# Performance work log

Hardware: AMD Instinct MI355X
Metric: run time of the kernel (lower is better)

The kernel has to match this reference:

```python
import jax, jax.numpy as jnp
import numpy as np

WIRE_DIM = 32
NUM_WIRES = 64
BATCH = 8192


def setup_inputs() -> dict:
    key = jax.random.key(0)
    k1, k2, k3, k4 = jax.random.split(key, 4)
    outputs = jax.random.normal(k1, (BATCH, NUM_WIRES * WIRE_DIM), dtype=jnp.float32)
    tests = jax.random.randint(k2, (BATCH, 2), 0, NUM_WIRES, dtype=jnp.int64)
    W1 = jax.random.normal(k3, (2 * WIRE_DIM, 10), dtype=jnp.float32) * 0.1
    b1 = jnp.zeros((10,), dtype=jnp.float32)
    W2 = jax.random.normal(k4, (10, 1), dtype=jnp.float32) * 0.1
    b2 = jnp.zeros((1,), dtype=jnp.float32)
    return {"outputs": outputs, "tests": tests, "W1": W1, "b1": b1, "W2": W2, "b2": b2}


def reference(outputs, tests, W1, b1, W2, b2):
    B = outputs.shape[0]
    W = outputs.shape[1] // WIRE_DIM          # num_wires
    wires = outputs.reshape(B, W, WIRE_DIM)   # [B, W, D]
    person = tests[:, 0]
    location = tests[:, 1]
    # gather_nd equivalent: person wire vector per batch element
    person_vec = wires[jnp.arange(B), person]                 # [B, D]
    # per-wire concat [person_vec, wire_vec] -> shared tiny MLP, vectorized over wires
    x = jnp.concatenate(
        [jnp.broadcast_to(person_vec[:, None, :], (B, W, WIRE_DIM)), wires], axis=-1
    )                                                          # [B, W, 2D]
    h = jax.nn.relu(jnp.einsum("bwd,dh->bwh", x, W1) + b1)     # [B, W, 10]
    logits = (jnp.einsum("bwh,ho->bwo", h, W2) + b2)[..., 0]   # [B, W]
    # sparse softmax cross entropy with location labels
    loss = -jnp.take_along_axis(jax.nn.log_softmax(logits, axis=-1),
                                location[:, None], axis=-1)[:, 0]  # [B]
    return loss
```

## Files before the change

kernel.cpp:

```cpp
#include <hip/hip_runtime.h>

#define WIRE_DIM  32
#define NUM_WIRES 64
#define BATCH     8192
#define HID       10
#define STRIDE    36

__device__ __forceinline__ float rl(float x, int slane) {
    return __uint_as_float(__builtin_amdgcn_readlane(__float_as_uint(x), slane));
}

__global__ __launch_bounds__(256) void isnet_kernel(
    const float* __restrict__ outputs,
    const int*   __restrict__ tests,
    const float* __restrict__ W1,
    const float* __restrict__ bias1,
    const float* __restrict__ W2,
    const float* __restrict__ bias2,
    float*       __restrict__ out)
{
    __shared__ __align__(16) float stage[4][NUM_WIRES * STRIDE];

    const int tid  = threadIdx.x;
    const int lane = tid & 63;
    const int wave = tid >> 6;
    float* buf = stage[wave];

    const int b = blockIdx.x * 4 + wave;

    const int sp = __builtin_amdgcn_readfirstlane(tests[2 * b]);
    const int sl = __builtin_amdgcn_readfirstlane(tests[2 * b + 1]);

    const int d  = lane & 31;
    const int h0 = (lane >> 5) * 5;
    float wp5[5];
    #pragma unroll
    for (int k = 0; k < 5; ++k) wp5[k] = W1[d * HID + h0 + k];

    const float* g = outputs + (size_t)b * (NUM_WIRES * WIRE_DIM) + lane * 4;
    const int r  = lane >> 3;
    const int cc = lane & 7;
    {
        float4 c[8];
        #pragma unroll
        for (int t = 0; t < 8; ++t) c[t] = *(const float4*)(g + t * 256);
        #pragma unroll
        for (int t = 0; t < 8; ++t)
            *(float4*)&buf[(t * 8 + r) * STRIDE + cc * 4] = c[t];
    }

    float pc[5];
    {
        const float pd = buf[sp * STRIDE + d];
        #pragma unroll
        for (int k = 0; k < 5; ++k) pc[k] = pd * wp5[k];
        #pragma unroll
        for (int off = 16; off > 0; off >>= 1)
            #pragma unroll
            for (int k = 0; k < 5; ++k) pc[k] += __shfl_xor(pc[k], off);
    }
    float pacc[HID];
    #pragma unroll
    for (int k = 0; k < 5; ++k) {
        pacc[k]     = rl(pc[k], 0);
        pacc[5 + k] = rl(pc[k], 32);
    }

    float4 x[8];
    #pragma unroll
    for (int t = 0; t < 8; ++t)
        x[t] = *(const float4*)&buf[lane * STRIDE + t * 4];

    float acc[HID];
    #pragma unroll
    for (int h = 0; h < HID; ++h) acc[h] = bias1[h] + pacc[h];

    #pragma unroll
    for (int j = 0; j < 8; ++j) {
        const float* ww = W1 + (32 + 4 * j) * HID;
        #pragma unroll
        for (int h = 0; h < HID; ++h) {
            acc[h] += x[j].x * ww[0 * HID + h] + x[j].y * ww[1 * HID + h]
                    + x[j].z * ww[2 * HID + h] + x[j].w * ww[3 * HID + h];
        }
    }

    float v = bias2[0];
    #pragma unroll
    for (int h = 0; h < HID; ++h) v += fmaxf(acc[h], 0.f) * W2[h];

    float m = v;
    #pragma unroll
    for (int off = 32; off > 0; off >>= 1) m = fmaxf(m, __shfl_xor(m, off));
    float s = __expf(v - m);
    #pragma unroll
    for (int off = 32; off > 0; off >>= 1) s += __shfl_xor(s, off);
    float lv = rl(v, sl);
    if (lane == 0) out[b] = m + __logf(s) - lv;
}

extern "C" void kernel_launch(void* const* d_in, const int* in_sizes, int n_in,
                              void* d_out, int out_size, void* d_ws, size_t ws_size,
                              hipStream_t stream) {
    const float* outputs = (const float*)d_in[0];
    const int*   tests   = (const int*)d_in[1];
    const float* W1      = (const float*)d_in[2];
    const float* b1      = (const float*)d_in[3];
    const float* W2      = (const float*)d_in[4];
    const float* b2      = (const float*)d_in[5];
    float* out = (float*)d_out;

    isnet_kernel<<<BATCH / 4, 256, 0, stream>>>(
        outputs, tests, W1, b1, W2, b2, out);
}
```

Baseline: 101.5 us.

## Process two batch rows per wave and drop softmax max-subtraction

```diff
diff --git a/kernel.cpp b/kernel.cpp
--- a/kernel.cpp
+++ b/kernel.cpp
@@ -26,10 +26,13 @@
     const int wave = tid >> 6;
     float* buf = stage[wave];
 
-    const int b = blockIdx.x * 4 + wave;
+    const int bA = blockIdx.x * 8 + wave * 2;
+    const int bB = bA + 1;
 
-    const int sp = __builtin_amdgcn_readfirstlane(tests[2 * b]);
-    const int sl = __builtin_amdgcn_readfirstlane(tests[2 * b + 1]);
+    const int spA = __builtin_amdgcn_readfirstlane(tests[2 * bA]);
+    const int slA = __builtin_amdgcn_readfirstlane(tests[2 * bA + 1]);
+    const int spB = __builtin_amdgcn_readfirstlane(tests[2 * bB]);
+    const int slB = __builtin_amdgcn_readfirstlane(tests[2 * bB + 1]);
 
     const int d  = lane & 31;
     const int h0 = (lane >> 5) * 5;
@@ -37,21 +40,29 @@
     #pragma unroll
     for (int k = 0; k < 5; ++k) wp5[k] = W1[d * HID + h0 + k];
 
-    const float* g = outputs + (size_t)b * (NUM_WIRES * WIRE_DIM) + lane * 4;
     const int r  = lane >> 3;
     const int cc = lane & 7;
-    {
-        float4 c[8];
-        #pragma unroll
-        for (int t = 0; t < 8; ++t) c[t] = *(const float4*)(g + t * 256);
-        #pragma unroll
-        for (int t = 0; t < 8; ++t)
-            *(float4*)&buf[(t * 8 + r) * STRIDE + cc * 4] = c[t];
-    }
+    const float* gA = outputs + (size_t)bA * (NUM_WIRES * WIRE_DIM) + lane * 4;
+    const float* gB = outputs + (size_t)bB * (NUM_WIRES * WIRE_DIM) + lane * 4;
+
+    float4 cA[8], cB[8];
+    #pragma unroll
+    for (int t = 0; t < 8; ++t) cA[t] = *(const float4*)(gA + t * 256);
+    #pragma unroll
+    for (int t = 0; t < 8; ++t) cB[t] = *(const float4*)(gB + t * 256);
+
+    #pragma unroll
+    for (int t = 0; t < 8; ++t)
+        *(float4*)&buf[(t * 8 + r) * STRIDE + cc * 4] = cA[t];
+
+    float4 x[8];
+    #pragma unroll
+    for (int t = 0; t < 8; ++t)
+        x[t] = *(const float4*)&buf[lane * STRIDE + t * 4];
 
     float pc[5];
     {
-        const float pd = buf[sp * STRIDE + d];
+        const float pd = buf[spA * STRIDE + d];
         #pragma unroll
         for (int k = 0; k < 5; ++k) pc[k] = pd * wp5[k];
         #pragma unroll
@@ -59,44 +70,69 @@
             #pragma unroll
             for (int k = 0; k < 5; ++k) pc[k] += __shfl_xor(pc[k], off);
     }
-    float pacc[HID];
+    float accA[HID];
     #pragma unroll
     for (int k = 0; k < 5; ++k) {
-        pacc[k]     = rl(pc[k], 0);
-        pacc[5 + k] = rl(pc[k], 32);
+        accA[k]     = bias1[k]     + rl(pc[k], 0);
+        accA[5 + k] = bias1[5 + k] + rl(pc[k], 32);
     }
-
-    float4 x[8];
-    #pragma unroll
-    for (int t = 0; t < 8; ++t)
-        x[t] = *(const float4*)&buf[lane * STRIDE + t * 4];
-
-    float acc[HID];
-    #pragma unroll
-    for (int h = 0; h < HID; ++h) acc[h] = bias1[h] + pacc[h];
-
     #pragma unroll
     for (int j = 0; j < 8; ++j) {
         const float* ww = W1 + (32 + 4 * j) * HID;
         #pragma unroll
-        for (int h = 0; h < HID; ++h) {
-            acc[h] += x[j].x * ww[0 * HID + h] + x[j].y * ww[1 * HID + h]
-                    + x[j].z * ww[2 * HID + h] + x[j].w * ww[3 * HID + h];
-        }
+        for (int h = 0; h < HID; ++h)
+            accA[h] += x[j].x * ww[h]           + x[j].y * ww[HID + h]
+                     + x[j].z * ww[2 * HID + h] + x[j].w * ww[3 * HID + h];
     }
+    float vA = bias2[0];
+    #pragma unroll
+    for (int h = 0; h < HID; ++h) vA += fmaxf(accA[h], 0.f) * W2[h];
+    float sA = __expf(vA);
+    #pragma unroll
+    for (int off = 32; off > 0; off >>= 1) sA += __shfl_xor(sA, off);
 
-    float v = bias2[0];
     #pragma unroll
-    for (int h = 0; h < HID; ++h) v += fmaxf(acc[h], 0.f) * W2[h];
+    for (int t = 0; t < 8; ++t)
+        *(float4*)&buf[(t * 8 + r) * STRIDE + cc * 4] = cB[t];
+    #pragma unroll
+    for (int t = 0; t < 8; ++t)
+        x[t] = *(const float4*)&buf[lane * STRIDE + t * 4];
+    {
+        const float pd = buf[spB * STRIDE + d];
+        #pragma unroll
+        for (int k = 0; k < 5; ++k) pc[k] = pd * wp5[k];
+        #pragma unroll
+        for (int off = 16; off > 0; off >>= 1)
+            #pragma unroll
+            for (int k = 0; k < 5; ++k) pc[k] += __shfl_xor(pc[k], off);
+    }
+    float accB[HID];
+    #pragma unroll
+    for (int k = 0; k < 5; ++k) {
+        accB[k]     = bias1[k]     + rl(pc[k], 0);
+        accB[5 + k] = bias1[5 + k] + rl(pc[k], 32);
+    }
+    #pragma unroll
+    for (int j = 0; j < 8; ++j) {
+        const float* ww = W1 + (32 + 4 * j) * HID;
+        #pragma unroll
+        for (int h = 0; h < HID; ++h)
+            accB[h] += x[j].x * ww[h]           + x[j].y * ww[HID + h]
+                     + x[j].z * ww[2 * HID + h] + x[j].w * ww[3 * HID + h];
+    }
+    float vB = bias2[0];
+    #pragma unroll
+    for (int h = 0; h < HID; ++h) vB += fmaxf(accB[h], 0.f) * W2[h];
+    float sB = __expf(vB);
+    #pragma unroll
+    for (int off = 32; off > 0; off >>= 1) sB += __shfl_xor(sB, off);
 
-    float m = v;
-    #pragma unroll
-    for (int off = 32; off > 0; off >>= 1) m = fmaxf(m, __shfl_xor(m, off));
-    float s = __expf(v - m);
-    #pragma unroll
-    for (int off = 32; off > 0; off >>= 1) s += __shfl_xor(s, off);
-    float lv = rl(v, sl);
-    if (lane == 0) out[b] = m + __logf(s) - lv;
+    const float lvA = rl(vA, slA);
+    const float lvB = rl(vB, slB);
+    if (lane == 0) {
+        out[bA] = __logf(sA) - lvA;
+        out[bB] = __logf(sB) - lvB;
+    }
 }
 
 extern "C" void kernel_launch(void* const* d_in, const int* in_sizes, int n_in,
@@ -110,6 +146,6 @@
     const float* b2      = (const float*)d_in[5];
     float* out = (float*)d_out;
 
-    isnet_kernel<<<BATCH / 4, 256, 0, stream>>>(
+    isnet_kernel<<<BATCH / 8, 256, 0, stream>>>(
         outputs, tests, W1, b1, W2, b2, out);
 }
```

After: 104.5 us. +2.9%, slower.
